# Performance work log

Measured on AMD Instinct MI355X. Metric: run time of the kernel, lower is better.

## Reference

```python
import jax, jax.numpy as jnp
import numpy as np

N_EMBED = 1024
N_HEAD = 16
HEAD_SIZE = N_EMBED // N_HEAD  # 64
SEQ = 2048
BATCH = 2
EPS = 1e-5


def setup_inputs() -> dict:
    key = jax.random.key(0)
    ks = jax.random.split(key, 16)
    s = lambda fan_in: 1.0 / np.sqrt(fan_in)
    d, h, hs, f = N_EMBED, N_HEAD, HEAD_SIZE, 4 * N_EMBED
    return {
        "x": jax.random.normal(ks[0], (BATCH, SEQ, d), dtype=jnp.float32),
        # per-head QKV projections (no bias), stacked over heads: [H, D, hs]
        "wq": jax.random.normal(ks[1], (h, d, hs), dtype=jnp.float32) * s(d),
        "wk": jax.random.normal(ks[2], (h, d, hs), dtype=jnp.float32) * s(d),
        "wv": jax.random.normal(ks[3], (h, d, hs), dtype=jnp.float32) * s(d),
        "w_proj": jax.random.normal(ks[4], (d, d), dtype=jnp.float32) * s(d),
        "b_proj": jnp.zeros((d,), dtype=jnp.float32),
        "w1": jax.random.normal(ks[5], (d, f), dtype=jnp.float32) * s(d),
        "b1": jnp.zeros((f,), dtype=jnp.float32),
        "w2": jax.random.normal(ks[6], (f, d), dtype=jnp.float32) * s(f),
        "b2": jnp.zeros((d,), dtype=jnp.float32),
        "g1": jnp.ones((d,), dtype=jnp.float32),
        "be1": jnp.zeros((d,), dtype=jnp.float32),
        "g2": jnp.ones((d,), dtype=jnp.float32),
        "be2": jnp.zeros((d,), dtype=jnp.float32),
    }


def _layer_norm(x, gamma, beta):
    mu = jnp.mean(x, axis=-1, keepdims=True)
    var = jnp.mean(jnp.square(x - mu), axis=-1, keepdims=True)
    return (x - mu) * jax.lax.rsqrt(var + EPS) * gamma + beta


def reference(x, wq, wk, wv, w_proj, b_proj, w1, b1, w2, b2, g1, be1, g2, be2):
    B, S, D = x.shape
    # per-head projections (vectorized over heads): [B, H, S, hs]
    q = jnp.einsum("bsd,hdk->bhsk", x, wq)
    k = jnp.einsum("bsd,hdk->bhsk", x, wk)
    v = jnp.einsum("bsd,hdk->bhsk", x, wv)
    scale = HEAD_SIZE ** -0.5
    scores = jnp.einsum("bhsk,bhtk->bhst", q, k) * scale  # [B,H,S,S]
    causal = jnp.tril(jnp.ones((S, S), dtype=bool))
    scores = jnp.where(causal, scores, -jnp.inf)
    w = jax.nn.softmax(scores, axis=-1)  # dropout=0 -> identity
    attn = jnp.einsum("bhst,bhtk->bhsk", w, v)  # [B,H,S,hs]
    # concat heads (head-major ordering matches torch.cat over heads)
    attn = attn.transpose(0, 2, 1, 3).reshape(B, S, D)
    y = attn @ w_proj + b_proj
    x = _layer_norm(x + y, g1, be1)
    y = jax.nn.relu(x @ w1 + b1) @ w2 + b2
    x = _layer_norm(x + y, g2, be2)
    return x
```

## Files before the change

kernel.cpp:

```cpp
#include <hip/hip_runtime.h>


typedef unsigned short u16;
typedef unsigned int u32;
typedef __attribute__((ext_vector_type(8))) short bf16x8;
typedef __attribute__((ext_vector_type(4))) float f32x4;
typedef __attribute__((ext_vector_type(2))) u32 u32x2;
typedef __attribute__((ext_vector_type(4))) _Float16 f16x4;

#define MFMA16(a, b, c) __builtin_amdgcn_mfma_f32_16x16x32_bf16(a, b, c, 0, 0, 0)
#define MFMAH(a, b, c) __builtin_amdgcn_mfma_f32_16x16x16f16(a, b, c, 0, 0, 0)

__device__ __forceinline__ u16 f2b(float f) {
  unsigned int u = __builtin_bit_cast(unsigned int, f);
  u = (u + 0x7fffu + ((u >> 16) & 1u)) >> 16;
  return (u16)u;
}

__device__ __forceinline__ void gload_lds16(const u16* g, u16* l) {
  __builtin_amdgcn_global_load_lds((const __attribute__((address_space(1))) void*)g,
                                   (__attribute__((address_space(3))) void*)l, 16, 0, 0);
}

__device__ __forceinline__ u32 pkrtz(float lo, float hi) {
  return __builtin_bit_cast(u32, __builtin_amdgcn_cvt_pkrtz(lo, hi));
}

__device__ __forceinline__ f16x4 pack4h(float a, float b, float c, float d) {
  u32x2 r = {pkrtz(a, b), pkrtz(c, d)};
  return __builtin_bit_cast(f16x4, r);
}

__device__ __forceinline__ u16 f2h(float v) {
  return __builtin_bit_cast(u16, (_Float16)v);
}


__global__ __launch_bounds__(256) void pack_all(
    const float* __restrict__ x, const float* __restrict__ wq,
    const float* __restrict__ wk, const float* __restrict__ wv,
    const float* __restrict__ wp, const float* __restrict__ w1,
    const float* __restrict__ w2, u16* __restrict__ Xbf, u16* __restrict__ WqkvT,
    u16* __restrict__ WprojT, u16* __restrict__ W1T, u16* __restrict__ W2T) {
  int bid = blockIdx.x;
  int t = threadIdx.x;
  if (bid >= 12288) {
    size_t i = ((size_t)(bid - 12288) * 256 + t) * 4;
    float4 v = *(const float4*)(x + i);
    Xbf[i + 0] = f2b(v.x);
    Xbf[i + 1] = f2b(v.y);
    Xbf[i + 2] = f2b(v.z);
    Xbf[i + 3] = f2b(v.w);
    return;
  }
  __shared__ float tile[32][33];
  int tx = t & 31, ty = t >> 5;
  const float* src;
  u16* dst;
  int R, C, r0, c0;
  float scale = 1.0f;
  if (bid < 3072) {
    int z = bid >> 6, q = bid & 63;
    int p = z >> 4, h = z & 15;
    src = (p == 0 ? wq : (p == 1 ? wk : wv)) + (size_t)h * 1024 * 64;
    scale = (p == 0) ? 0.1803368801f : 1.0f;
    dst = WqkvT + (size_t)(p * 1024 + h * 64) * 1024;
    R = 1024; C = 64;
    c0 = (q & 1) * 32; r0 = (q >> 1) * 32;
  } else if (bid < 4096) {
    int q = bid - 3072;
    src = wp; dst = WprojT; R = 1024; C = 1024;
    c0 = (q & 31) * 32; r0 = (q >> 5) * 32;
  } else if (bid < 8192) {
    int q = bid - 4096;
    src = w1; dst = W1T; R = 1024; C = 4096;
    c0 = (q & 127) * 32; r0 = (q >> 7) * 32;
  } else {
    int q = bid - 8192;
    src = w2; dst = W2T; R = 4096; C = 1024;
    c0 = (q & 31) * 32; r0 = (q >> 5) * 32;
  }
#pragma unroll
  for (int i = 0; i < 4; ++i)
    tile[ty + i * 8][tx] = src[(size_t)(r0 + ty + i * 8) * C + c0 + tx];
  __syncthreads();
#pragma unroll
  for (int i = 0; i < 4; ++i)
    dst[(size_t)(c0 + ty + i * 8) * R + r0 + tx] = f2b(tile[tx][ty + i * 8] * scale);
}


template <int MODE>
__global__ __launch_bounds__(256, 4) void gemm_bf16(const u16* __restrict__ A,
                                                    const u16* __restrict__ Bt, int M,
                                                    int N, int Kc, int lda,
                                                    const float* __restrict__ bias,
                                                    u16* __restrict__ outB, int ldc,
                                                    u16* __restrict__ vtg) {
  constexpr int BM = 128, BN = 128, BK = 64;
  constexpr int IM = 4, JN = 4;
  __shared__ u16 As[BM * BK];
  __shared__ u16 Bs[BN * BK];
  int t = threadIdx.x;
  int m0 = blockIdx.x * BM, n0 = blockIdx.y * BN;
  int kb = blockIdx.z * Kc;
  int lane = t & 63, wid = t >> 6;
  int wm = (wid >> 1) * 64, wn = (wid & 1) * 64;
  int m16 = lane & 15, quad = lane >> 4;
  int sw = m16 & 7;

  f32x4 acc[IM][JN] = {};

  for (int k0 = kb; k0 < kb + Kc; k0 += BK) {
    __syncthreads();
#pragma unroll
    for (int i = 0; i < 4; ++i) {
      int S = i * 256 + t;
      int row = S >> 3, c = S & 7;
      gload_lds16(&A[(size_t)(m0 + row) * lda + k0 + (c ^ (row & 7)) * 8],
                  &As[(i * 256 + wid * 64) * 8]);
    }
#pragma unroll
    for (int i = 0; i < 4; ++i) {
      int S = i * 256 + t;
      int row = S >> 3, c = S & 7;
      gload_lds16(&Bt[(size_t)(n0 + row) * lda + k0 + (c ^ (row & 7)) * 8],
                  &Bs[(i * 256 + wid * 64) * 8]);
    }
    __syncthreads();
#pragma unroll
    for (int kk = 0; kk < 2; ++kk) {
      bf16x8 af[IM], bfr[JN];
      int slot = (kk * 4 + quad) ^ sw;
#pragma unroll
      for (int i = 0; i < IM; ++i)
        af[i] = *(const bf16x8*)&As[(wm + i * 16 + m16) * BK + slot * 8];
#pragma unroll
      for (int j = 0; j < JN; ++j)
        bfr[j] = *(const bf16x8*)&Bs[(wn + j * 16 + m16) * BK + slot * 8];
#pragma unroll
      for (int i = 0; i < IM; ++i)
#pragma unroll
        for (int j = 0; j < JN; ++j) acc[i][j] = MFMA16(af[i], bfr[j], acc[i][j]);
    }
  }

  if (MODE == 3 && n0 >= 2048) {
#pragma unroll
    for (int i = 0; i < IM; ++i)
#pragma unroll
      for (int j = 0; j < JN; ++j) {
        int dg = n0 + wn + j * 16 + m16 - 2048;
        int hh = dg >> 6, dd = dg & 63;
        int token = m0 + wm + i * 16 + quad * 4;
        int bb = token >> 11, tt = token & 2047;
        u32x2 pv = {pkrtz(acc[i][j][0], acc[i][j][1]),
                    pkrtz(acc[i][j][2], acc[i][j][3])};
        *(u32x2*)&vtg[(((size_t)bb * 16 + hh) * 64 + dd) * 2048 + tt] = pv;
      }
    return;
  }

  u16* pb = (MODE == 4) ? outB + (size_t)blockIdx.z * M * N : outB;
#pragma unroll
  for (int i = 0; i < IM; ++i)
#pragma unroll
    for (int j = 0; j < JN; ++j) {
      int col = n0 + wn + j * 16 + m16;
      float bv = (MODE == 1) ? bias[col] : 0.0f;
#pragma unroll
      for (int r = 0; r < 4; ++r) {
        int row = m0 + wm + i * 16 + quad * 4 + r;
        float v = acc[i][j][r];
        if (MODE == 1) {
          v += bv;
          v = v > 0.0f ? v : 0.0f;
          pb[(size_t)row * ldc + col] = f2b(v);
        } else if (MODE == 4) {
          pb[(size_t)row * ldc + col] = f2h(v);
        } else {
          pb[(size_t)row * ldc + col] = f2b(v);
        }
      }
    }
}


__constant__ unsigned char R_QB[32] = {7, 6, 11, 11, 5, 10, 10, 9, 9, 4, 8,
                                       8, 3, 15, 15, 15, 15, 14, 14, 14, 13, 13,
                                       13, 13, 12, 12, 12, 2, 14, 12, 1, 0};
__constant__ unsigned char R_K0[32] = {0, 0, 0, 12, 0, 0, 11, 0, 10, 0, 0,
                                       9, 0, 0, 8, 16, 24, 0, 8, 16, 0, 7,
                                       14, 21, 0, 7, 14, 0, 24, 21, 0, 0};
__constant__ unsigned char R_NIT[32] = {16, 14, 12, 12, 12, 11, 11, 10, 10, 10, 9,
                                        9, 8, 8, 8, 8, 8, 8, 8, 8, 7, 7,
                                        7, 7, 7, 7, 7, 6, 6, 5, 4, 2};
__constant__ unsigned char R_ST[32] = {255, 255, 6, 7, 255, 4, 5, 2, 3, 255, 0,
                                       1, 255, 20, 21, 22, 23, 16, 17, 18, 12, 13,
                                       14, 15, 8, 9, 10, 255, 19, 11, 255, 255};
__constant__ unsigned char CB_BASE[8] = {0, 2, 4, 6, 8, 12, 16, 20};

__global__ __launch_bounds__(256) void attn_part(const u16* __restrict__ qk,
                                                 const u16* __restrict__ vtg,
                                                 u16* __restrict__ attn_out,
                                                 u16* __restrict__ opart,
                                                 float2* __restrict__ ml) {
  int rank = blockIdx.x >> 5, bh = blockIdx.x & 31;
  int qb = R_QB[rank];
  int k_start = R_K0[rank] * 64;
  int iters = R_NIT[rank];
  int st = R_ST[rank];
  int b = bh >> 4, h = bh & 15;

  int t = threadIdx.x, lane = t & 63, w = t >> 6;
  int m16 = lane & 15, quad = lane >> 4;
  int wq0 = qb * 128 + w * 32;

  __shared__ u16 Ks[2][64 * 64];
  __shared__ u16 Vs[2][64 * 64];

  bf16x8 qa[2][2];
#pragma unroll
  for (int qs = 0; qs < 2; ++qs) {
    const u16* qp = qk + (size_t)(b * 2048 + wq0 + qs * 16 + m16) * 2048 + h * 64;
    qa[qs][0] = *(const bf16x8*)&qp[quad * 8];
    qa[qs][1] = *(const bf16x8*)&qp[32 + quad * 8];
  }

  f32x4 oT[2][4] = {};
  f32x4 lacc[2] = {};
  float mrun[2] = {-1e30f, -1e30f};

  int row0 = t >> 3, c0 = t & 7;
  int row1 = 32 + row0;
  const u16* kbase = qk + (size_t)(b * 2048) * 2048 + 1024 + h * 64;
  const u16* vbase = vtg + ((size_t)(b * 16 + h) * 64) * 2048;
  int sw = m16 & 7;

#define STAGE_ASYNC(T0, BUF)                                                        \
  {                                                                                 \
    gload_lds16(&kbase[(size_t)((T0) + row0) * 2048 + (c0 ^ (row0 & 7)) * 8],       \
                &Ks[BUF][(w * 64) * 8]);                                            \
    gload_lds16(&kbase[(size_t)((T0) + row1) * 2048 + (c0 ^ (row1 & 7)) * 8],       \
                &Ks[BUF][(256 + w * 64) * 8]);                                      \
    gload_lds16(&vbase[(size_t)row0 * 2048 + (T0) + (c0 ^ (row0 & 7)) * 8],         \
                &Vs[BUF][(w * 64) * 8]);                                            \
    gload_lds16(&vbase[(size_t)row1 * 2048 + (T0) + (c0 ^ (row1 & 7)) * 8],         \
                &Vs[BUF][(256 + w * 64) * 8]);                                      \
  }

  STAGE_ASYNC(k_start, 0);
  __syncthreads();

  for (int it = 0; it < iters; ++it) {
    int t0 = k_start + it * 64;
    int cur = it & 1;
    if (it + 1 < iters) STAGE_ASYNC(t0 + 64, !cur);

    if (t0 <= wq0 + 31) {
      f32x4 sv[2][4];
#pragma unroll
      for (int ts = 0; ts < 4; ++ts) {
        bf16x8 ka0 = *(const bf16x8*)&Ks[cur][(ts * 16 + m16) * 64 + (quad ^ sw) * 8];
        bf16x8 ka1 =
            *(const bf16x8*)&Ks[cur][(ts * 16 + m16) * 64 + ((4 + quad) ^ sw) * 8];
#pragma unroll
        for (int qs = 0; qs < 2; ++qs) {
          f32x4 a = {};
          a = MFMA16(ka0, qa[qs][0], a);
          a = MFMA16(ka1, qa[qs][1], a);
          sv[qs][ts] = a;
        }
      }
      if (t0 + 63 > wq0) {
#pragma unroll
        for (int qs = 0; qs < 2; ++qs)
#pragma unroll
          for (int ts = 0; ts < 4; ++ts)
#pragma unroll
            for (int rr = 0; rr < 4; ++rr) {
              int key = t0 + ts * 16 + quad * 4 + rr;
              if (key > wq0 + qs * 16 + m16) sv[qs][ts][rr] = -3e38f;
            }
      }
#pragma unroll
      for (int qs = 0; qs < 2; ++qs) {
        float mx = fmaxf(fmaxf(sv[qs][0][0], sv[qs][0][1]),
                         fmaxf(sv[qs][0][2], sv[qs][0][3]));
#pragma unroll
        for (int ts = 1; ts < 4; ++ts)
          mx = fmaxf(mx, fmaxf(fmaxf(sv[qs][ts][0], sv[qs][ts][1]),
                               fmaxf(sv[qs][ts][2], sv[qs][ts][3])));
        mx = fmaxf(mx, __shfl_xor(mx, 16));
        mx = fmaxf(mx, __shfl_xor(mx, 32));
        float mnew = fmaxf(mrun[qs], mx);
        float alpha = exp2f(mrun[qs] - mnew);
        mrun[qs] = mnew;
        lacc[qs] *= alpha;
#pragma unroll
        for (int ds = 0; ds < 4; ++ds) oT[qs][ds] *= alpha;
      }
      f16x4 pf[2][4];
#pragma unroll
      for (int qs = 0; qs < 2; ++qs)
#pragma unroll
        for (int ts = 0; ts < 4; ++ts) {
          float p0 = exp2f(sv[qs][ts][0] - mrun[qs]);
          float p1 = exp2f(sv[qs][ts][1] - mrun[qs]);
          float p2 = exp2f(sv[qs][ts][2] - mrun[qs]);
          float p3 = exp2f(sv[qs][ts][3] - mrun[qs]);
          lacc[qs][0] += p0;
          lacc[qs][1] += p1;
          lacc[qs][2] += p2;
          lacc[qs][3] += p3;
          pf[qs][ts] = pack4h(p0, p1, p2, p3);
        }
#pragma unroll
      for (int ts = 0; ts < 4; ++ts)
#pragma unroll
        for (int ds = 0; ds < 4; ++ds) {
          f16x4 av = __builtin_bit_cast(
              f16x4, *(const u32x2*)&Vs[cur][(ds * 16 + m16) * 64 +
                                             (((ts * 2 + (quad >> 1)) ^ sw) * 8) +
                                             (quad & 1) * 4]);
          oT[0][ds] = MFMAH(av, pf[0][ts], oT[0][ds]);
          oT[1][ds] = MFMAH(av, pf[1][ts], oT[1][ds]);
        }
    }
    __syncthreads();
  }
#undef STAGE_ASYNC

  if (st == 255) {
#pragma unroll
    for (int qs = 0; qs < 2; ++qs) {
      float ls = lacc[qs][0] + lacc[qs][1] + lacc[qs][2] + lacc[qs][3];
      ls += __shfl_xor(ls, 16);
      ls += __shfl_xor(ls, 32);
      float rl = 1.0f / ls;
      int q = wq0 + qs * 16 + m16;
#pragma unroll
      for (int ds = 0; ds < 4; ++ds) {
        f32x4 o = oT[qs][ds];
        u32x2 ov = {(u32)f2b(o[0] * rl) | ((u32)f2b(o[1] * rl) << 16),
                    (u32)f2b(o[2] * rl) | ((u32)f2b(o[3] * rl) << 16)};
        *(u32x2*)&attn_out[(size_t)(b * 2048 + q) * 1024 + h * 64 + ds * 16 +
                           quad * 4] = ov;
      }
    }
  } else {
    size_t sbase = ((size_t)st * 32 + bh) * 128;
#pragma unroll
    for (int qs = 0; qs < 2; ++qs) {
      float ls = lacc[qs][0] + lacc[qs][1] + lacc[qs][2] + lacc[qs][3];
      ls += __shfl_xor(ls, 16);
      ls += __shfl_xor(ls, 32);
      int qloc = w * 32 + qs * 16 + m16;
#pragma unroll
      for (int ds = 0; ds < 4; ++ds) {
        f32x4 o = oT[qs][ds];
        u32x2 ov = {pkrtz(o[0], o[1]), pkrtz(o[2], o[3])};
        *(u32x2*)&opart[(sbase + qloc) * 64 + ds * 16 + quad * 4] = ov;
      }
      if (quad == 0) ml[sbase + qloc] = make_float2(mrun[qs], ls);
    }
  }
}

__global__ __launch_bounds__(256) void attn_comb(const u16* __restrict__ opart,
                                                 const float2* __restrict__ ml,
                                                 u16* __restrict__ attn_out) {
  int qb = 8 + blockIdx.x, bh = blockIdx.y;
  int b = bh >> 4, h = bh & 15;
  int nseg = (qb < 12) ? 2 : 4;
  int base = CB_BASE[qb - 8];
  int t = threadIdx.x;
  int q = t >> 1, dh = (t & 1) * 32;

  float m[4], l[4], wgt[4];
  float M = -3e38f;
  for (int s = 0; s < nseg; ++s) {
    float2 v = ml[((size_t)(base + s) * 32 + bh) * 128 + q];
    m[s] = v.x;
    l[s] = v.y;
    M = fmaxf(M, v.x);
  }
  float lsum = 0.0f;
  for (int s = 0; s < nseg; ++s) {
    wgt[s] = exp2f(m[s] - M);
    lsum += wgt[s] * l[s];
  }
  float rl = 1.0f / lsum;

  size_t orow = (size_t)(b * 2048 + qb * 128 + q) * 1024 + h * 64 + dh;
#pragma unroll 2
  for (int dd = 0; dd < 32; dd += 4) {
    float o0 = 0, o1 = 0, o2 = 0, o3 = 0;
    for (int s = 0; s < nseg; ++s) {
      f16x4 hv = __builtin_bit_cast(
          f16x4, *(const u32x2*)&opart[(((size_t)(base + s) * 32 + bh) * 128 + q) * 64 +
                                       dh + dd]);
      o0 += wgt[s] * (float)hv[0];
      o1 += wgt[s] * (float)hv[1];
      o2 += wgt[s] * (float)hv[2];
      o3 += wgt[s] * (float)hv[3];
    }
    u32x2 ov = {(u32)f2b(o0 * rl) | ((u32)f2b(o1 * rl) << 16),
                (u32)f2b(o2 * rl) | ((u32)f2b(o3 * rl) << 16)};
    *(u32x2*)&attn_out[orow + dd] = ov;
  }
}


__global__ __launch_bounds__(256) void ln_comb(const u16* __restrict__ parts, int np,
                                               const float* __restrict__ bias,
                                               const float* __restrict__ resid,
                                               const float* __restrict__ g,
                                               const float* __restrict__ be,
                                               float* __restrict__ outF,
                                               u16* __restrict__ outB) {
  int row = blockIdx.x;
  int t = threadIdx.x;
  size_t off = (size_t)row * 1024 + t * 4;
  float4 bv4 = *(const float4*)(bias + t * 4);
  float a0 = bv4.x, a1 = bv4.y, a2 = bv4.z, a3 = bv4.w;
  for (int c = 0; c < np; ++c) {
    f16x4 hv =
        __builtin_bit_cast(f16x4, *(const u32x2*)&parts[(size_t)c * 4096 * 1024 + off]);
    a0 += (float)hv[0];
    a1 += (float)hv[1];
    a2 += (float)hv[2];
    a3 += (float)hv[3];
  }
  float4 rv = *(const float4*)(resid + off);
  a0 += rv.x;
  a1 += rv.y;
  a2 += rv.z;
  a3 += rv.w;

  float s = a0 + a1 + a2 + a3;
  float sq = a0 * a0 + a1 * a1 + a2 * a2 + a3 * a3;
#pragma unroll
  for (int d = 1; d < 64; d <<= 1) {
    s += __shfl_xor(s, d);
    sq += __shfl_xor(sq, d);
  }
  __shared__ float red[8];
  int lane = t & 63, wid = t >> 6;
  if (lane == 0) {
    red[wid] = s;
    red[4 + wid] = sq;
  }
  __syncthreads();
  s = red[0] + red[1] + red[2] + red[3];
  sq = red[4] + red[5] + red[6] + red[7];
  float mu = s * (1.0f / 1024.0f);
  float var = sq * (1.0f / 1024.0f) - mu * mu;
  float rstd = rsqrtf(var + 1e-5f);
  float4 gv = *(const float4*)(g + t * 4);
  float4 bev = *(const float4*)(be + t * 4);
  float o0 = (a0 - mu) * rstd * gv.x + bev.x;
  float o1 = (a1 - mu) * rstd * gv.y + bev.y;
  float o2 = (a2 - mu) * rstd * gv.z + bev.z;
  float o3 = (a3 - mu) * rstd * gv.w + bev.w;
  if (outF) {
    float4 ov = {o0, o1, o2, o3};
    *(float4*)(outF + off) = ov;
  }
  if (outB) {
    outB[off + 0] = f2b(o0);
    outB[off + 1] = f2b(o1);
    outB[off + 2] = f2b(o2);
    outB[off + 3] = f2b(o3);
  }
}


extern "C" void kernel_launch(void* const* d_in, const int* in_sizes, int n_in,
                              void* d_out, int out_size, void* d_ws, size_t ws_size,
                              hipStream_t stream) {
  const float* x = (const float*)d_in[0];
  const float* wq = (const float*)d_in[1];
  const float* wk = (const float*)d_in[2];
  const float* wv = (const float*)d_in[3];
  const float* w_proj = (const float*)d_in[4];
  const float* b_proj = (const float*)d_in[5];
  const float* w1 = (const float*)d_in[6];
  const float* b1 = (const float*)d_in[7];
  const float* w2 = (const float*)d_in[8];
  const float* b2 = (const float*)d_in[9];
  const float* g1 = (const float*)d_in[10];
  const float* be1 = (const float*)d_in[11];
  const float* g2 = (const float*)d_in[12];
  const float* be2 = (const float*)d_in[13];
  float* out = (float*)d_out;

  const int M = 4096;
  char* w = (char*)d_ws;
  u16* Xbf = (u16*)w;        w += (size_t)M * 1024 * 2;
  u16* WqkvT = (u16*)w;      w += (size_t)3072 * 1024 * 2;
  u16* WprojT = (u16*)w;     w += (size_t)1024 * 1024 * 2;
  u16* W1T = (u16*)w;        w += (size_t)4096 * 1024 * 2;
  u16* X1b = (u16*)w;        w += (size_t)M * 1024 * 2;
  u16* W2T = (u16*)w;        w += (size_t)1024 * 4096 * 2;
  u16* QK = (u16*)w;         w += (size_t)M * 2048 * 2;
  u16* Vtg = (u16*)w;        w += (size_t)2 * 16 * 64 * 2048 * 2;
  u16* Attn = (u16*)w;       w += (size_t)M * 1024 * 2;
  float* X1f = (float*)w;    w += (size_t)M * 1024 * 4;

  u16* Pdown = Xbf;
  u16* Pproj = QK;
  u16* Hbuf = QK;
  u16* Opart = (u16*)X1f;
  float2* Ml = (float2*)((char*)X1f + (size_t)13 * 1024 * 1024);

  pack_all<<<16384, 256, 0, stream>>>(x, wq, wk, wv, w_proj, w1, w2, Xbf, WqkvT,
                                      WprojT, W1T, W2T);

  gemm_bf16<3><<<dim3(32, 24, 1), 256, 0, stream>>>(Xbf, WqkvT, M, 3072, 1024, 1024,
                                                    nullptr, QK, 2048, Vtg);

  attn_part<<<1024, 256, 0, stream>>>(QK, Vtg, Attn, Opart, Ml);
  attn_comb<<<dim3(8, 32), 256, 0, stream>>>(Opart, Ml, Attn);

  gemm_bf16<4><<<dim3(32, 8, 2), 256, 0, stream>>>(Attn, WprojT, M, 1024, 512, 1024,
                                                   nullptr, Pproj, 1024, nullptr);
  ln_comb<<<M, 256, 0, stream>>>(Pproj, 2, b_proj, x, g1, be1, X1f, X1b);

  gemm_bf16<1><<<dim3(32, 32, 1), 256, 0, stream>>>(X1b, W1T, M, 4096, 1024, 1024, b1,
                                                    Hbuf, 4096, nullptr);

  gemm_bf16<4><<<dim3(32, 8, 4), 256, 0, stream>>>(Hbuf, W2T, M, 1024, 1024, 4096,
                                                   nullptr, Pdown, 1024, nullptr);
  ln_comb<<<M, 256, 0, stream>>>(Pdown, 4, b2, X1f, g2, be2, out, nullptr);
}
```

Measured before the change: 337.2 us.

## Rebalance split-KV attention into 40 ranks with lazy rescale and MFMA priority

Re-partitions the causal attention work into 40 ranks per head with at most 8 key tiles each, up from 32 ranks with up to 16. More query blocks are split across segments, so the combine kernel now handles 12 query blocks with 2–4 segments, and partial outputs spill into a second workspace buffer. It also skips the online-softmax rescale unless the running max grows by more than a threshold, raises wave priority around the MFMA sections, and sets an occupancy hint in launch bounds. The finer split aims to shrink the tail from long ranks, at the cost of more partial-output traffic and combine work, with some fp16 overflow risk from the lazy rescale.

After: 458.1 us. 1.36x slower.

```diff
diff --git a/kernel.cpp b/kernel.cpp
--- a/kernel.cpp
+++ b/kernel.cpp
@@ -186,25 +186,34 @@
 }
 
 
-__constant__ unsigned char R_QB[32] = {7, 6, 11, 11, 5, 10, 10, 9, 9, 4, 8,
-                                       8, 3, 15, 15, 15, 15, 14, 14, 14, 13, 13,
-                                       13, 13, 12, 12, 12, 2, 14, 12, 1, 0};
-__constant__ unsigned char R_K0[32] = {0, 0, 0, 12, 0, 0, 11, 0, 10, 0, 0,
-                                       9, 0, 0, 8, 16, 24, 0, 8, 16, 0, 7,
-                                       14, 21, 0, 7, 14, 0, 24, 21, 0, 0};
-__constant__ unsigned char R_NIT[32] = {16, 14, 12, 12, 12, 11, 11, 10, 10, 10, 9,
-                                        9, 8, 8, 8, 8, 8, 8, 8, 8, 7, 7,
-                                        7, 7, 7, 7, 7, 6, 6, 5, 4, 2};
-__constant__ unsigned char R_ST[32] = {255, 255, 6, 7, 255, 4, 5, 2, 3, 255, 0,
-                                       1, 255, 20, 21, 22, 23, 16, 17, 18, 12, 13,
-                                       14, 15, 8, 9, 10, 255, 19, 11, 255, 255};
-__constant__ unsigned char CB_BASE[8] = {0, 2, 4, 6, 8, 12, 16, 20};
-
-__global__ __launch_bounds__(256) void attn_part(const u16* __restrict__ qk,
-                                                 const u16* __restrict__ vtg,
-                                                 u16* __restrict__ attn_out,
-                                                 u16* __restrict__ opart,
-                                                 float2* __restrict__ ml) {
+__constant__ unsigned char R_QB[40] = {
+    15, 15, 15, 15, 14, 14, 11, 11, 11, 10, 7,  7,  3,
+    14, 14, 13, 13, 13, 13, 12, 12, 10, 10, 9,  9,  6,  6,
+    12, 12, 9,  8,  8,  8,  5,  5,  2,
+    4,  4,  1,  0};
+__constant__ unsigned char R_K0[40] = {
+    0,  8,  16, 24, 0,  8,  0,  8,  16, 0,  0,  8,  0,
+    16, 23, 0,  7,  14, 21, 0,  7,  8,  15, 0,  7,  0,  7,
+    14, 20, 14, 0,  6,  12, 0,  6,  0,
+    0,  5,  0,  0};
+__constant__ unsigned char R_NIT[40] = {
+    8, 8, 8, 8, 8, 8, 8, 8, 8, 8, 8, 8, 8,
+    7, 7, 7, 7, 7, 7, 7, 7, 7, 7, 7, 7, 7, 7,
+    6, 6, 6, 6, 6, 6, 6, 6, 6,
+    5, 5, 4, 2};
+__constant__ unsigned char R_ST[40] = {
+    32, 33, 34, 35, 28, 29, 17, 18, 19, 14, 6,  7,  255,
+    30, 31, 24, 25, 26, 27, 20, 21, 15, 16, 11, 12, 4,  5,
+    22, 23, 13, 8,  9,  10, 2,  3,  255,
+    0,  1,  255, 255};
+__constant__ unsigned char CB_BASE[12] = {0, 2, 4, 6, 8, 11, 14, 17, 20, 24, 28, 32};
+
+__global__ __launch_bounds__(256, 5) void attn_part(const u16* __restrict__ qk,
+                                                    const u16* __restrict__ vtg,
+                                                    u16* __restrict__ attn_out,
+                                                    u16* __restrict__ opart0,
+                                                    u16* __restrict__ opart1,
+                                                    float2* __restrict__ ml) {
   int rank = blockIdx.x >> 5, bh = blockIdx.x & 31;
   int qb = R_QB[rank];
   int k_start = R_K0[rank] * 64;
@@ -259,6 +268,7 @@
 
     if (t0 <= wq0 + 31) {
       f32x4 sv[2][4];
+      __builtin_amdgcn_s_setprio(1);
 #pragma unroll
       for (int ts = 0; ts < 4; ++ts) {
         bf16x8 ka0 = *(const bf16x8*)&Ks[cur][(ts * 16 + m16) * 64 + (quad ^ sw) * 8];
@@ -272,6 +282,7 @@
           sv[qs][ts] = a;
         }
       }
+      __builtin_amdgcn_s_setprio(0);
       if (t0 + 63 > wq0) {
 #pragma unroll
         for (int qs = 0; qs < 2; ++qs)
@@ -293,12 +304,14 @@
                                fmaxf(sv[qs][ts][2], sv[qs][ts][3])));
         mx = fmaxf(mx, __shfl_xor(mx, 16));
         mx = fmaxf(mx, __shfl_xor(mx, 32));
-        float mnew = fmaxf(mrun[qs], mx);
-        float alpha = exp2f(mrun[qs] - mnew);
-        mrun[qs] = mnew;
-        lacc[qs] *= alpha;
-#pragma unroll
-        for (int ds = 0; ds < 4; ++ds) oT[qs][ds] *= alpha;
+        if (!__all(mx <= mrun[qs] + 6.0f)) {
+          float mnew = fmaxf(mrun[qs], mx);
+          float alpha = exp2f(mrun[qs] - mnew);
+          mrun[qs] = mnew;
+          lacc[qs] *= alpha;
+#pragma unroll
+          for (int ds = 0; ds < 4; ++ds) oT[qs][ds] *= alpha;
+        }
       }
       f16x4 pf[2][4];
 #pragma unroll
@@ -315,6 +328,7 @@
           lacc[qs][3] += p3;
           pf[qs][ts] = pack4h(p0, p1, p2, p3);
         }
+      __builtin_amdgcn_s_setprio(1);
 #pragma unroll
       for (int ts = 0; ts < 4; ++ts)
 #pragma unroll
@@ -326,6 +340,7 @@
           oT[0][ds] = MFMAH(av, pf[0][ts], oT[0][ds]);
           oT[1][ds] = MFMAH(av, pf[1][ts], oT[1][ds]);
         }
+      __builtin_amdgcn_s_setprio(0);
     }
     __syncthreads();
   }
@@ -349,7 +364,16 @@
       }
     }
   } else {
-    size_t sbase = ((size_t)st * 32 + bh) * 128;
+    u16* po;
+    size_t sb;
+    if (st < 32) {
+      po = opart0;
+      sb = ((size_t)st * 32 + bh) * 128;
+    } else {
+      po = opart1;
+      sb = ((size_t)(st - 32) * 32 + bh) * 128;
+    }
+    size_t mlb = ((size_t)st * 32 + bh) * 128;
 #pragma unroll
     for (int qs = 0; qs < 2; ++qs) {
       float ls = lacc[qs][0] + lacc[qs][1] + lacc[qs][2] + lacc[qs][3];
@@ -360,20 +384,21 @@
       for (int ds = 0; ds < 4; ++ds) {
         f32x4 o = oT[qs][ds];
         u32x2 ov = {pkrtz(o[0], o[1]), pkrtz(o[2], o[3])};
-        *(u32x2*)&opart[(sbase + qloc) * 64 + ds * 16 + quad * 4] = ov;
-      }
-      if (quad == 0) ml[sbase + qloc] = make_float2(mrun[qs], ls);
-    }
-  }
-}
-
-__global__ __launch_bounds__(256) void attn_comb(const u16* __restrict__ opart,
+        *(u32x2*)&po[(sb + qloc) * 64 + ds * 16 + quad * 4] = ov;
+      }
+      if (quad == 0) ml[mlb + qloc] = make_float2(mrun[qs], ls);
+    }
+  }
+}
+
+__global__ __launch_bounds__(256) void attn_comb(const u16* __restrict__ opart0,
+                                                 const u16* __restrict__ opart1,
                                                  const float2* __restrict__ ml,
                                                  u16* __restrict__ attn_out) {
-  int qb = 8 + blockIdx.x, bh = blockIdx.y;
+  int qb = 4 + blockIdx.x, bh = blockIdx.y;
   int b = bh >> 4, h = bh & 15;
-  int nseg = (qb < 12) ? 2 : 4;
-  int base = CB_BASE[qb - 8];
+  int nseg = (qb < 8) ? 2 : (qb < 12 ? 3 : 4);
+  int base = CB_BASE[qb - 4];
   int t = threadIdx.x;
   int q = t >> 1, dh = (t & 1) * 32;
 
@@ -392,14 +417,21 @@
   }
   float rl = 1.0f / lsum;
 
-  size_t orow = (size_t)(b * 2048 + qb * 128 + q) * 1024 + h * 64 + dh;
+  constexpr size_t SLOT = (size_t)32 * 128 * 64;
+  const u16* orow[4];
+  for (int s = 0; s < nseg; ++s) {
+    int sa = base + s;
+    const u16* bp =
+        (sa < 32) ? opart0 + (size_t)sa * SLOT : opart1 + (size_t)(sa - 32) * SLOT;
+    orow[s] = bp + ((size_t)bh * 128 + q) * 64 + dh;
+  }
+
+  size_t oout = (size_t)(b * 2048 + qb * 128 + q) * 1024 + h * 64 + dh;
 #pragma unroll 2
   for (int dd = 0; dd < 32; dd += 4) {
     float o0 = 0, o1 = 0, o2 = 0, o3 = 0;
     for (int s = 0; s < nseg; ++s) {
-      f16x4 hv = __builtin_bit_cast(
-          f16x4, *(const u32x2*)&opart[(((size_t)(base + s) * 32 + bh) * 128 + q) * 64 +
-                                       dh + dd]);
+      f16x4 hv = __builtin_bit_cast(f16x4, *(const u32x2*)&orow[s][dd]);
       o0 += wgt[s] * (float)hv[0];
       o1 += wgt[s] * (float)hv[1];
       o2 += wgt[s] * (float)hv[2];
@@ -407,7 +439,7 @@
     }
     u32x2 ov = {(u32)f2b(o0 * rl) | ((u32)f2b(o1 * rl) << 16),
                 (u32)f2b(o2 * rl) | ((u32)f2b(o3 * rl) << 16)};
-    *(u32x2*)&attn_out[orow + dd] = ov;
+    *(u32x2*)&attn_out[oout + dd] = ov;
   }
 }
 
@@ -511,8 +543,9 @@
   u16* Pdown = Xbf;
   u16* Pproj = QK;
   u16* Hbuf = QK;
-  u16* Opart = (u16*)X1f;
-  float2* Ml = (float2*)((char*)X1f + (size_t)13 * 1024 * 1024);
+  u16* Opart0 = (u16*)X1f;
+  u16* Opart1 = Xbf;
+  float2* Ml = (float2*)((char*)d_ws + (size_t)4 * 1024 * 1024);
 
   pack_all<<<16384, 256, 0, stream>>>(x, wq, wk, wv, w_proj, w1, w2, Xbf, WqkvT,
                                       WprojT, W1T, W2T);
@@ -520,8 +553,8 @@
   gemm_bf16<3><<<dim3(32, 24, 1), 256, 0, stream>>>(Xbf, WqkvT, M, 3072, 1024, 1024,
                                                     nullptr, QK, 2048, Vtg);
 
-  attn_part<<<1024, 256, 0, stream>>>(QK, Vtg, Attn, Opart, Ml);
-  attn_comb<<<dim3(8, 32), 256, 0, stream>>>(Opart, Ml, Attn);
+  attn_part<<<1280, 256, 0, stream>>>(QK, Vtg, Attn, Opart0, Opart1, Ml);
+  attn_comb<<<dim3(12, 32), 256, 0, stream>>>(Opart0, Opart1, Ml, Attn);
 
   gemm_bf16<4><<<dim3(32, 8, 2), 256, 0, stream>>>(Attn, WprojT, M, 1024, 512, 1024,
                                                    nullptr, Pproj, 1024, nullptr);
```
